# Performance work log

Hardware: AMD Instinct MI355X
Metric: run time of the kernel (lower is better)

The kernel has to match this reference:

```python
import jax, jax.numpy as jnp
import numpy as np

MAX_DISP = 48


def setup_inputs() -> dict:
    key = jax.random.key(0)
    k1, k2 = jax.random.split(key)
    b, c, h, w = 2, 32, 96, 320
    left_feature = jax.random.normal(k1, (b, c, h, w), dtype=jnp.float32)
    right_feature = jax.random.normal(k2, (b, c, h, w), dtype=jnp.float32)
    return {"left_feature": left_feature, "right_feature": right_feature}


def reference(left_feature, right_feature):
    # volume[b, c, d, h, w] = left[b, c, h, w] - right[b, c, h, w - d]  if w >= d else 0
    b, c, h, w = left_feature.shape
    d_idx = jnp.arange(MAX_DISP)[:, None]          # [D, 1]
    w_idx = jnp.arange(w)[None, :]                 # [1, W]
    src = w_idx - d_idx                            # [D, W] source column in right feature
    valid = src >= 0                               # [D, W]
    src_c = jnp.clip(src, 0, w - 1)
    # gather shifted right feature: [b, c, h, D, W] -> [b, c, D, h, W]
    right_shift = right_feature[:, :, :, src_c].transpose(0, 1, 3, 2, 4)
    diff = left_feature[:, :, None, :, :] - right_shift
    volume = jnp.where(valid[None, None, :, None, :], diff, jnp.float32(0))
    return volume
```

## Files before the change

### kernel.cpp

```cpp
#include <hip/hip_runtime.h>

#define BB 2
#define CC 32
#define HH 96
#define WW 320
#define DD 48
#define W4 (WW / 4)

__global__ __launch_bounds__(256) void diffvol_kernel(
        const float* __restrict__ left,
        const float* __restrict__ right,
        float* __restrict__ out) {
    int idx = blockIdx.x * blockDim.x + threadIdx.x;

    int x4 = idx % W4;
    int t  = idx / W4;
    int y  = t % HH;
    t /= HH;
    int d  = t % DD;
    int bc = t / DD;

    int base = (bc * HH + y) * WW;
    int x = x4 * 4;

    const float4 lv = *(const float4*)(left + base + x);
    const float* rrow = right + base;

    float4 o;
    o.x = (x + 0 >= d) ? lv.x - rrow[x + 0 - d] : 0.0f;
    o.y = (x + 1 >= d) ? lv.y - rrow[x + 1 - d] : 0.0f;
    o.z = (x + 2 >= d) ? lv.z - rrow[x + 2 - d] : 0.0f;
    o.w = (x + 3 >= d) ? lv.w - rrow[x + 3 - d] : 0.0f;

    ((float4*)out)[idx] = o;
}

extern "C" void kernel_launch(void* const* d_in, const int* in_sizes, int n_in,
                              void* d_out, int out_size, void* d_ws, size_t ws_size,
                              hipStream_t stream) {
    const float* left  = (const float*)d_in[0];
    const float* right = (const float*)d_in[1];
    float* out = (float*)d_out;

    const int total4 = BB * CC * DD * HH * W4;
    const int block = 256;
    const int grid = total4 / block;
    diffvol_kernel<<<grid, block, 0, stream>>>(left, right, out);
}
```

Measured before the change: 466.8 us.

## Stage right row in shared memory and loop over disparities per block

Each block now handles one (batch*channel, row) pair. It loads the left value and the right row into shared memory once, then writes all 48 disparity slices from that data. This removes the repeated global reads of left and right for every disparity and the per-element index math. In exchange, stores become scalar instead of float4 and the grid is much smaller, with more work per thread. A branch skips the validity check for columns 64 and above.

```diff
diff --git a/kernel.cpp b/kernel.cpp
--- a/kernel.cpp
+++ b/kernel.cpp
@@ -5,34 +5,37 @@
 #define HH 96
 #define WW 320
 #define DD 48
-#define W4 (WW / 4)
 
-__global__ __launch_bounds__(256) void diffvol_kernel(
+__global__ __launch_bounds__(320) void diffvol_kernel(
         const float* __restrict__ left,
         const float* __restrict__ right,
         float* __restrict__ out) {
-    int idx = blockIdx.x * blockDim.x + threadIdx.x;
+    __shared__ float rrow[WW];
 
-    int x4 = idx % W4;
-    int t  = idx / W4;
-    int y  = t % HH;
-    t /= HH;
-    int d  = t % DD;
-    int bc = t / DD;
+    const int tid = threadIdx.x;
+    const int blk = blockIdx.x;
+    const int y   = blk % HH;
+    const int bc  = blk / HH;
 
-    int base = (bc * HH + y) * WW;
-    int x = x4 * 4;
+    const int base = (bc * HH + y) * WW;
+    const float lv = left[base + tid];
+    rrow[tid] = right[base + tid];
+    __syncthreads();
 
-    const float4 lv = *(const float4*)(left + base + x);
-    const float* rrow = right + base;
+    float* o = out + ((bc * DD) * HH + y) * WW + tid;
+    const int dstride = HH * WW;
 
-    float4 o;
-    o.x = (x + 0 >= d) ? lv.x - rrow[x + 0 - d] : 0.0f;
-    o.y = (x + 1 >= d) ? lv.y - rrow[x + 1 - d] : 0.0f;
-    o.z = (x + 2 >= d) ? lv.z - rrow[x + 2 - d] : 0.0f;
-    o.w = (x + 3 >= d) ? lv.w - rrow[x + 3 - d] : 0.0f;
-
-    ((float4*)out)[idx] = o;
+    if (tid >= 64) {
+        #pragma unroll
+        for (int d = 0; d < DD; ++d) {
+            o[d * dstride] = lv - rrow[tid - d];
+        }
+    } else {
+        #pragma unroll
+        for (int d = 0; d < DD; ++d) {
+            o[d * dstride] = (tid >= d) ? lv - rrow[tid - d] : 0.0f;
+        }
+    }
 }
 
 extern "C" void kernel_launch(void* const* d_in, const int* in_sizes, int n_in,
@@ -42,8 +45,6 @@
     const float* right = (const float*)d_in[1];
     float* out = (float*)d_out;
 
-    const int total4 = BB * CC * DD * HH * W4;
-    const int block = 256;
-    const int grid = total4 / block;
-    diffvol_kernel<<<grid, block, 0, stream>>>(left, right, out);
+    const int grid = BB * CC * HH;
+    diffvol_kernel<<<grid, 320, 0, stream>>>(left, right, out);
 }
```

Result: faster. 388.4 us (-16.8%).
